# Performance work log

Measured on AMD Instinct MI355X. Metric: run time of the kernel, lower is better.

Reference implementation:

```python
import jax, jax.numpy as jnp
import numpy as np

# ---- static config (mirrors LSSTransform defaults) ----
B, N, CIN, CT = 4, 6, 512, 64
OGH, OGW, DS = 256, 704, 16
FH, FW = OGH // DS, OGW // DS            # 16, 44
DB0, DB1, DBS = 4.0, 45.0, 1.0
D = int((DB1 - DB0) / DBS)               # 41 depth bins
NXX, NYY, NZZ = 128, 128, 1              # BEV grid from x/y/z bounds
DXv = np.array([0.8, 0.8, 20.0], np.float32)            # dx
BXv = np.array([-51.2 + 0.4, -51.2 + 0.4, 0.0], np.float32)  # bx = lower + dx/2


def _frustum():
    # (D, fH, fW, 3) of (pixel_u, pixel_v, depth), as in create_frustum
    ds = np.broadcast_to(np.arange(DB0, DB1, DBS, dtype=np.float32)[:, None, None], (D, FH, FW))
    xs = np.broadcast_to(np.linspace(0, OGW - 1, FW, dtype=np.float32)[None, None, :], (D, FH, FW))
    ys = np.broadcast_to(np.linspace(0, OGH - 1, FH, dtype=np.float32)[None, :, None], (D, FH, FW))
    return jnp.asarray(np.stack([xs, ys, ds], axis=-1))

FRUSTUM = _frustum()


def setup_inputs() -> dict:
    key = jax.random.key(0)
    k0, k1, k2 = jax.random.split(key, 3)
    x = jax.random.normal(k0, (B, N, CIN, FH, FW), jnp.float32)
    # camera->ego rotation: ego = (z_cam, x_cam, y_cam), so depth maps to ego-x
    R = jnp.array([[0., 0., 1.], [1., 0., 0.], [0., 1., 0.]], jnp.float32)
    rots = jnp.broadcast_to(R, (B, N, 3, 3)) + 0.0
    trans = 0.5 * jax.random.normal(k1, (B, N, 3), jnp.float32)
    K = jnp.array([[500., 0., OGW / 2.], [0., 500., OGH / 2.], [0., 0., 1.]], jnp.float32)
    intrins = jnp.broadcast_to(K, (B, N, 3, 3)) + 0.0
    post_rots = jnp.broadcast_to(jnp.eye(3, dtype=jnp.float32), (B, N, 3, 3)) + 0.0
    post_trans = jnp.zeros((B, N, 3), jnp.float32)
    Wd = 0.02 * jax.random.normal(k2, (D + CT, CIN), jnp.float32)  # depthnet 1x1 conv weight
    bd = jnp.zeros((D + CT,), jnp.float32)
    return dict(x=x, rots=rots, trans=trans, intrins=intrins,
                post_rots=post_rots, post_trans=post_trans, Wd=Wd, bd=bd)


def _forward(x, rots, trans, intrins, post_rots, post_trans, Wd, bd):
    # depthnet: 1x1 conv == channel matmul
    feat = jnp.einsum('bnchw,oc->bnohw', x, Wd) + bd[None, None, :, None, None]
    depth = jax.nn.softmax(feat[:, :, :D], axis=2)          # (B,N,D,H,W)
    cvt = feat[:, :, D:D + CT]                              # (B,N,CT,H,W)
    vol = depth[:, :, None] * cvt[:, :, :, None]            # (B,N,CT,D,H,W)
    vol = jnp.transpose(vol, (0, 1, 3, 4, 5, 2))            # (B,N,D,H,W,CT)

    # get_geometry: undo image augs, unproject, cam->ego
    pts = FRUSTUM[None, None] - post_trans[:, :, None, None, None, :]
    pts = jnp.einsum('bnij,bndhwj->bndhwi', jnp.linalg.inv(post_rots), pts)
    pts = jnp.concatenate([pts[..., :2] * pts[..., 2:3], pts[..., 2:3]], axis=-1)
    comb = rots @ jnp.linalg.inv(intrins)
    pts = jnp.einsum('bnij,bndhwj->bndhwi', comb, pts) + trans[:, :, None, None, None, :]

    # voxel_pooling: truncating cast matches torch .long()
    g = ((pts - (jnp.asarray(BXv) - jnp.asarray(DXv) / 2.0)) / jnp.asarray(DXv)).astype(jnp.int32)
    gx, gy, gz = g[..., 0], g[..., 1], g[..., 2]
    kept = (gx >= 0) & (gx < NXX) & (gy >= 0) & (gy < NYY) & (gz >= 0) & (gz < NZZ)
    bix = jnp.arange(B, dtype=jnp.int32)[:, None, None, None, None]
    vox = ((bix * NZZ + gz) * NYY + gy) * NXX + gx          # flat voxel id per point
    TOT = B * NZZ * NYY * NXX
    seg = jnp.where(kept, vox, TOT).reshape(-1)             # invalid -> trash bucket
    feats = vol.reshape(-1, CT)                             # (Nprime, CT)
    sums = jax.ops.segment_sum(feats, seg, num_segments=TOT + 1)[:TOT]
    final = sums.reshape(B, NZZ, NYY, NXX, CT)
    # (B, C, nz, ny, nx) then cat over z into channels -> (B, nz*C, ny, nx)
    final = jnp.transpose(final, (0, 1, 4, 2, 3)).reshape(B, NZZ * CT, NYY, NXX)
    return final


def reference(x, rots, trans, intrins, post_rots, post_trans, Wd, bd):
    return _forward(x, rots, trans, intrins, post_rots, post_trans, Wd, bd)
```

## Files before the change

### kernel.cpp

```cpp
#include <hip/hip_runtime.h>
#include <hip/hip_bf16.h>
#include <math.h>

#define B_   4
#define N_   6
#define CIN  512
#define CT   64
#define Dd   41
#define FH   16
#define FW   44
#define NPIX 704
#define NO   105
#define DSTR 48
#define NXX  128
#define NYY  128
#define NZZ  1
#define TOT  (B_*NZZ*NYY*NXX)
#define NPTS (B_*N_*Dd*NPIX)
#define NCHUNK ((NPTS+63)/64)

#define WSTRIDE 520

#define GEMM_BLOCKS 1056
#define GEOM_BLOCKS 4224

typedef __attribute__((ext_vector_type(8))) short short8;
typedef __attribute__((ext_vector_type(4))) float f32x4;


__device__ __forceinline__ unsigned short f2bf(float f) {
    unsigned u = __float_as_uint(f);
    u += 0x7FFFu + ((u >> 16) & 1u);
    return (unsigned short)(u >> 16);
}

__device__ __forceinline__ void inv3(const double* m, double* o) {
    double a=m[0],b=m[1],c=m[2],d=m[3],e=m[4],f=m[5],g=m[6],h=m[7],i=m[8];
    double A  =  (e*i - f*h);
    double Bc = -(d*i - f*g);
    double Cc =  (d*h - e*g);
    double det = a*A + b*Bc + c*Cc;
    double inv = 1.0/det;
    o[0]=A*inv;            o[1]=-(b*i - c*h)*inv;  o[2]= (b*f - c*e)*inv;
    o[3]=Bc*inv;           o[4]= (a*i - c*g)*inv;  o[5]=-(a*f - c*d)*inv;
    o[6]=Cc*inv;           o[7]=-(a*h - b*g)*inv;  o[8]= (a*e - b*d)*inv;
}

__device__ __forceinline__ void geom_lane(const double* s_tf, int b, int pix, int l,
                                          bool& kept, int& vox) {
    const int hh = pix / FW, ww = pix % FW;
    const double fx = (double)((float)(ww * (703.0/43.0)));
    const double fy = (double)((float)(hh * 17.0));
    const double px = fx - s_tf[21], py = fy - s_tf[22], mz = -s_tf[23];
    const double qx0 = s_tf[ 9]*px + s_tf[10]*py + s_tf[11]*mz, qx1 = s_tf[11];
    const double qy0 = s_tf[12]*px + s_tf[13]*py + s_tf[14]*mz, qy1 = s_tf[14];
    const double qz0 = s_tf[15]*px + s_tf[16]*py + s_tf[17]*mz, qz1 = s_tf[17];
    const double ux0 = s_tf[0]*qx0 + s_tf[1]*qy0 + s_tf[2], ux1 = s_tf[0]*qx1 + s_tf[1]*qy1;
    const double uy0 = s_tf[3]*qx0 + s_tf[4]*qy0 + s_tf[5], uy1 = s_tf[3]*qx1 + s_tf[4]*qy1;
    const double uz0 = s_tf[6]*qx0 + s_tf[7]*qy0 + s_tf[8], uz1 = s_tf[6]*qx1 + s_tf[7]*qy1;
    const double t0 = s_tf[18], t1 = s_tf[19], t2 = s_tf[20];

    const double DXD = (double)0.8f;
    const double LOX = (double)(-50.8f) - DXD*0.5;
    const double LOY = LOX;
    const double DZD = 20.0;
    const double LOZ = -10.0;

    kept = false; vox = 0;
    if (l < Dd) {
        double fz = 4.0 + (double)l;
        double qz = qz0 + qz1*fz;
        double sx = qz*(ux0 + ux1*fz) + t0;
        double sy = qz*(uy0 + uy1*fz) + t1;
        double sz = qz*(uz0 + uz1*fz) + t2;
        int gx = (int)((sx - LOX) / DXD);
        int gy = (int)((sy - LOY) / DXD);
        int gz = (int)((sz - LOZ) / DZD);
        kept = (gx>=0) & (gx<NXX) & (gy>=0) & (gy<NYY) & (gz>=0) & (gz<NZZ);
        vox  = (((b*NZZ + gz)*NYY + gy)*NXX + gx);
    }
}

__global__ __launch_bounds__(256) void prep_kernel(
    const float* __restrict__ rots, const float* __restrict__ trans,
    const float* __restrict__ intrins, const float* __restrict__ post_rots,
    const float* __restrict__ post_trans, const float* __restrict__ Wd,
    const float* __restrict__ x,
    double* __restrict__ tf, unsigned short* __restrict__ WdB,
    unsigned short* __restrict__ xB)
{
    const int t = threadIdx.x;
    if (blockIdx.x < 2112) {
        __shared__ float s_x[64*65];
        const int p    = blockIdx.x;
        const int bn   = p / 88;
        const int r    = p % 88;
        const int kg   = r / 11;
        const int tile = r % 11;
        const int pix0 = tile * 64;

        const float* src = x + ((size_t)bn*CIN + kg*64)*NPIX + pix0;
        #pragma unroll
        for (int i = 0; i < 16; i++) {
            int idx = i*256 + t;
            int k  = idx >> 6;
            int px = idx & 63;
            s_x[k*65 + px] = src[(size_t)k*NPIX + px];
        }
        __syncthreads();

        const int px  = t & 63;
        #pragma unroll
        for (int pass = 0; pass < 2; pass++) {
            int k8l = (t >> 6) + 4*pass;
            unsigned pk[4];
            #pragma unroll
            for (int i = 0; i < 4; i++) {
                float a = s_x[(k8l*8 + 2*i    )*65 + px];
                float c = s_x[(k8l*8 + 2*i + 1)*65 + px];
                pk[i] = (unsigned)f2bf(a) | ((unsigned)f2bf(c) << 16);
            }
            unsigned* dst = (unsigned*)&xB[(((size_t)(bn*64 + kg*8 + k8l))*NPIX + pix0 + px)*8];
            *(uint4*)dst = make_uint4(pk[0], pk[1], pk[2], pk[3]);
        }
    } else {
        int b2 = blockIdx.x - 2112;
        int idx = b2*256 + t;
        if (idx < 128*CIN) {
            int o = idx / CIN;
            WdB[idx] = (o < NO) ? f2bf(Wd[idx]) : (unsigned short)0;
        }
        if (b2 == 0 && t < B_*N_) {
            int bn = t;
            double k[9], pr[9], r[9], ik[9], ipr[9], c[9];
            for (int i=0;i<9;i++) { k[i]=intrins[bn*9+i]; pr[i]=post_rots[bn*9+i]; r[i]=rots[bn*9+i]; }
            inv3(k, ik);
            inv3(pr, ipr);
            for (int i=0;i<3;i++)
                for (int j=0;j<3;j++) {
                    double s = 0.0;
                    for (int kk=0;kk<3;kk++) s += r[i*3+kk]*ik[kk*3+j];
                    c[i*3+j] = s;
                }
            double* o = tf + bn*24;
            for (int i=0;i<9;i++) o[i]   = c[i];
            for (int i=0;i<9;i++) o[9+i] = ipr[i];
            for (int i=0;i<3;i++) o[18+i] = (double)trans[bn*3+i];
            for (int i=0;i<3;i++) o[21+i] = (double)post_trans[bn*3+i];
        }
    }
}

__global__ __launch_bounds__(256) void gemm_geom_kernel(
    const unsigned short* __restrict__ xB, const unsigned short* __restrict__ WdB,
    const float* __restrict__ bd, const double* __restrict__ tf,
    float* __restrict__ featD, float* __restrict__ featB,
    int* __restrict__ hist, int* __restrict__ rank_arr)
{
    __shared__ unsigned short s_wd[32*WSTRIDE];
    __shared__ double s_tf[24];

    const int t    = threadIdx.x;
    const int l    = t & 63;
    const int wv   = t >> 6;

    if (blockIdx.x < GEMM_BLOCKS) {
        const int col  = l & 15;
        const int quad = l >> 4;
        const int xcd = blockIdx.x & 7;
        const int q   = blockIdx.x >> 3;
        const int s   = q & 3;
        const int pg  = q >> 2;
        const int p   = pg*8 + xcd;
        const int bn   = p / 11;
        const int tile = p % 11;
        const int pix0 = tile * 64;

        {
            const int o  = t >> 3;
            const int c8 = t & 7;
            const unsigned short* srcw = WdB + (size_t)(s*32 + o)*CIN;
            #pragma unroll
            for (int i = 0; i < 8; i++) {
                int k = c8*8 + i*64;
                *(uint4*)&s_wd[o*WSTRIDE + k] = *(const uint4*)&srcw[k];
            }
        }
        __syncthreads();

        f32x4 acc[2];
        acc[0] = (f32x4){0.f,0.f,0.f,0.f};
        acc[1] = (f32x4){0.f,0.f,0.f,0.f};

        const int pix = pix0 + wv*16 + col;
        const unsigned short* xbase = xB + (((size_t)(bn*64))*NPIX)*8;

        #pragma unroll
        for (int ks = 0; ks < 16; ks++) {
            const int k8 = ks*4 + quad;
            short8 bfr = *(const short8*)&xbase[((size_t)k8*NPIX + pix)*8];
            #pragma unroll
            for (int j = 0; j < 2; j++) {
                short8 afr = *(const short8*)&s_wd[(j*16 + col)*WSTRIDE + ks*32 + quad*8];
                acc[j] = __builtin_amdgcn_mfma_f32_16x16x32_bf16(afr, bfr, acc[j], 0, 0, 0);
            }
        }

        const size_t prow = (size_t)(bn*NPIX + pix);
        #pragma unroll
        for (int j = 0; j < 2; j++) {
            #pragma unroll
            for (int rr = 0; rr < 4; rr++) {
                int o = (2*s + j)*16 + quad*4 + rr;
                if (o < Dd) {
                    featD[prow*DSTR + o] = acc[j][rr] + bd[o];
                } else if (o < NO) {
                    featB[prow*CT + (o - Dd)] = acc[j][rr] + bd[o];
                }
            }
        }
    } else {
        const int bid2 = blockIdx.x - GEMM_BLOCKS;
        const int bid  = (bid2 & 7) * 528 + (bid2 >> 3);
        const int bn  = bid / 176;
        const int pix = (bid % 176)*4 + wv;
        const int b   = bn / N_;

        if (t < 24) s_tf[t] = tf[bn*24 + t];
        __syncthreads();

        bool kept; int vox;
        geom_lane(s_tf, b, pix, l, kept, vox);
        if (kept) {
            int rank = atomicAdd(&hist[vox], 1);
            rank_arr[(size_t)(bn*NPIX + pix)*Dd + l] = rank;
        }
    }
}

__global__ __launch_bounds__(256) void scan1_kernel(const int* __restrict__ hist,
                                                    int* __restrict__ offs,
                                                    int* __restrict__ bsum) {
    __shared__ int s[256];
    const int t = threadIdx.x;
    const int i = blockIdx.x*256 + t;
    int val = hist[i];
    s[t] = val;
    __syncthreads();
    #pragma unroll
    for (int off = 1; off < 256; off <<= 1) {
        int u = (t >= off) ? s[t-off] : 0;
        __syncthreads();
        s[t] += u;
        __syncthreads();
    }
    offs[i] = s[t] - val;
    if (t == 255) bsum[blockIdx.x] = s[255];
}

__global__ __launch_bounds__(256) void scan2_kernel(int* __restrict__ bsum,
                                                    int* __restrict__ np) {
    __shared__ int s[256];
    const int t = threadIdx.x;
    int v = bsum[t];
    s[t] = v;
    __syncthreads();
    #pragma unroll
    for (int off = 1; off < 256; off <<= 1) {
        int u = (t >= off) ? s[t-off] : 0;
        __syncthreads();
        s[t] += u;
        __syncthreads();
    }
    bsum[t] = s[t] - v;
    if (t == 255) np[0] = s[255];
}

__global__ __launch_bounds__(256) void sm_scatter_kernel(
    const float* __restrict__ featD, const double* __restrict__ tf,
    const int* __restrict__ offs, const int* __restrict__ bsum,
    const int* __restrict__ rank_arr, uint2* __restrict__ rec)
{
    __shared__ double s_tf[24];
    const int bid = (blockIdx.x & 7) * 528 + (blockIdx.x >> 3);
    const int t   = threadIdx.x;
    const int l   = t & 63;
    const int wv  = t >> 6;
    const int bn  = bid / 176;
    const int pix = (bid % 176)*4 + wv;
    const int b   = bn / N_;

    if (t < 24) s_tf[t] = tf[bn*24 + t];
    __syncthreads();

    const size_t prow = (size_t)(bn*NPIX + pix);

    float logit = (l < Dd) ? featD[prow*DSTR + l] : -3.0e38f;
    float mm = logit;
    #pragma unroll
    for (int off = 32; off > 0; off >>= 1) mm = fmaxf(mm, __shfl_xor(mm, off));
    float e = (l < Dd) ? expf(logit - mm) : 0.0f;
    float ssum = e;
    #pragma unroll
    for (int off = 32; off > 0; off >>= 1) ssum += __shfl_xor(ssum, off);
    const float wgt = e / ssum;

    bool kept; int vox;
    geom_lane(s_tf, b, pix, l, kept, vox);
    if (kept) {
        int pos = offs[vox] + bsum[vox >> 8] + rank_arr[prow*Dd + l];
        unsigned pk = ((unsigned)vox << 15) | (unsigned)prow;
        rec[pos] = make_uint2(pk, __float_as_uint(wgt));
    }
}

__global__ __launch_bounds__(256) void gather_kernel(
    const uint2* __restrict__ rec, const int* __restrict__ np,
    const float* __restrict__ featB, float* __restrict__ scat)
{
    const int bid = (blockIdx.x & 7) * 339 + (blockIdx.x >> 3);
    const int t  = threadIdx.x;
    const int wv = t >> 6;
    const int l  = t & 63;
    const int chunk = bid * 4 + wv;
    const int base  = chunk * 64;
    const int Np = np[0];
    if (base >= Np) return;
    int cnt = Np - base; if (cnt > 64) cnt = 64;

    unsigned pk = 0; float w = 0.0f;
    if (l < cnt) { uint2 r = rec[base + l]; pk = r.x; w = __uint_as_float(r.y); }
    unsigned pkm = __shfl(pk, (l == 0) ? 0 : (l - 1));
    unsigned long long starts =
        __ballot((l > 0) && (l < cnt) && ((pk >> 15) != (pkm >> 15)));

    unsigned long long m = starts;
    int rs = 0;
    while (rs < cnt) {
        int re = m ? (__ffsll((unsigned long long)m) - 1) : cnt;
        if (m) m &= m - 1;
        float acc = 0.0f;
        for (int j = rs; j < re; j++) {
            unsigned pkj = __shfl(pk, j);
            float    wj  = __shfl(w, j);
            unsigned id  = pkj & 0x7FFFu;
            acc += wj * featB[(size_t)id * CT + l];
        }
        unsigned vrun = __shfl(pk, rs) >> 15;
        float* dst = scat + (size_t)vrun * CT + l;
        if (rs == 0 || re == cnt) {
            unsafeAtomicAdd(dst, acc);
        } else {
            *dst = acc;
        }
        rs = re;
    }
}

__global__ __launch_bounds__(256) void transpose_k(const float* __restrict__ scat,
                                                   float* __restrict__ out) {
    __shared__ float tile[64][65];
    int b  = blockIdx.x >> 8;
    int t0 = (blockIdx.x & 255) * 64;
    const float* src = scat + (size_t)b * (NYY*NXX) * CT;
    #pragma unroll
    for (int i=0;i<16;i++) {
        int idx = threadIdx.x + i*256;
        int p = idx >> 6, c = idx & 63;
        tile[p][c] = src[(size_t)(t0+p)*CT + c];
    }
    __syncthreads();
    float* dst = out + (size_t)b * CT * (NYY*NXX);
    #pragma unroll
    for (int i=0;i<16;i++) {
        int idx = threadIdx.x + i*256;
        int c = idx >> 6, p = idx & 63;
        dst[(size_t)c*(NYY*NXX) + t0 + p] = tile[p][c];
    }
}

extern "C" void kernel_launch(void* const* d_in, const int* in_sizes, int n_in,
                              void* d_out, int out_size, void* d_ws, size_t ws_size,
                              hipStream_t stream) {
    const float* x          = (const float*)d_in[0];
    const float* rots       = (const float*)d_in[1];
    const float* trans      = (const float*)d_in[2];
    const float* intrins    = (const float*)d_in[3];
    const float* post_rots  = (const float*)d_in[4];
    const float* post_trans = (const float*)d_in[5];
    const float* Wd         = (const float*)d_in[6];
    const float* bd         = (const float*)d_in[7];
    float* out = (float*)d_out;

    char* ws = (char*)d_ws;
    float*          featB  = (float*)ws;          ws += (size_t)B_*N_*NPIX*CT*4;
    float*          featD  = (float*)ws;          ws += (size_t)B_*N_*NPIX*DSTR*4;
    char*           Xreg   = ws;                  ws += (size_t)B_*N_*CIN*NPIX*2;
    int*            rank_a = (int*)ws;            ws += (size_t)NPTS*4;
    uint2*          rec    = (uint2*)ws;          ws += (size_t)NPTS*8;
    int*            hist   = (int*)ws;            ws += (size_t)TOT*4;
    int*            offs   = (int*)ws;            ws += (size_t)TOT*4;
    int*            bsum   = (int*)ws;            ws += 256*4;
    int*            np     = (int*)ws;            ws += 256;
    double*         tf     = (double*)ws;         ws += (size_t)B_*N_*24*8;
    unsigned short* WdB    = (unsigned short*)ws; ws += (size_t)128*CIN*2;

    unsigned short* xB   = (unsigned short*)Xreg;
    float*          scat = (float*)Xreg;

    hipMemsetAsync(hist, 0, (size_t)TOT*4, stream);
    prep_kernel<<<2368, 256, 0, stream>>>(rots, trans, intrins, post_rots, post_trans,
                                          Wd, x, tf, WdB, xB);
    gemm_geom_kernel<<<GEMM_BLOCKS + GEOM_BLOCKS, 256, 0, stream>>>(
        xB, WdB, bd, tf, featD, featB, hist, rank_a);
    hipMemsetAsync(scat, 0, (size_t)TOT*CT*4, stream);
    scan1_kernel<<<TOT/256, 256, 0, stream>>>(hist, offs, bsum);
    scan2_kernel<<<1, 256, 0, stream>>>(bsum, np);
    sm_scatter_kernel<<<B_*N_*176, 256, 0, stream>>>(featD, tf, offs, bsum, rank_a, rec);
    gather_kernel<<<2712, 256, 0, stream>>>(rec, np, featB, scat);
    transpose_k<<<B_*(NYY*NXX/64), 256, 0, stream>>>(scat, out);
}
```

Before: 208.9 us.

## Interleave GEMM and geometry blocks, read weights from global, vectorize prep loads

The fused GEMM and geometry kernel now interleaves one GEMM block per five blocks instead of running all GEMM blocks first, so the compute-bound MFMA work overlaps with the atomic-bound geometry work. The GEMM blocks no longer stage the weight slice in shared memory and read A fragments straight from global or L2, which removes the large LDS allocation and a barrier but adds redundant global loads. The prep transpose now uses float4 loads with a padded stride of 68, and since 64*1056=4224*... mapping bid2 = bidx - bidx/5 - 1 covers geometry blocks exactly (5280 = 1056*5).

```diff
diff --git a/kernel.cpp b/kernel.cpp
--- a/kernel.cpp
+++ b/kernel.cpp
@@ -19,10 +19,9 @@
 #define NPTS (B_*N_*Dd*NPIX)
 #define NCHUNK ((NPTS+63)/64)
 
-#define WSTRIDE 520
-
 #define GEMM_BLOCKS 1056
 #define GEOM_BLOCKS 4224
+#define FUSED_BLOCKS (GEMM_BLOCKS + GEOM_BLOCKS)
 
 typedef __attribute__((ext_vector_type(8))) short short8;
 typedef __attribute__((ext_vector_type(4))) float f32x4;
@@ -91,7 +90,7 @@
 {
     const int t = threadIdx.x;
     if (blockIdx.x < 2112) {
-        __shared__ float s_x[64*65];
+        __shared__ float s_x[64*68];
         const int p    = blockIdx.x;
         const int bn   = p / 88;
         const int r    = p % 88;
@@ -101,11 +100,12 @@
 
         const float* src = x + ((size_t)bn*CIN + kg*64)*NPIX + pix0;
         #pragma unroll
-        for (int i = 0; i < 16; i++) {
+        for (int i = 0; i < 4; i++) {
             int idx = i*256 + t;
-            int k  = idx >> 6;
-            int px = idx & 63;
-            s_x[k*65 + px] = src[(size_t)k*NPIX + px];
+            int k   = idx >> 4;
+            int px4 = (idx & 15) * 4;
+            float4 v = *(const float4*)&src[(size_t)k*NPIX + px4];
+            *(float4*)&s_x[k*68 + px4] = v;
         }
         __syncthreads();
 
@@ -116,8 +116,8 @@
             unsigned pk[4];
             #pragma unroll
             for (int i = 0; i < 4; i++) {
-                float a = s_x[(k8l*8 + 2*i    )*65 + px];
-                float c = s_x[(k8l*8 + 2*i + 1)*65 + px];
+                float a = s_x[(k8l*8 + 2*i    )*68 + px];
+                float c = s_x[(k8l*8 + 2*i + 1)*68 + px];
                 pk[i] = (unsigned)f2bf(a) | ((unsigned)f2bf(c) << 16);
             }
             unsigned* dst = (unsigned*)&xB[(((size_t)(bn*64 + kg*8 + k8l))*NPIX + pix0 + px)*8];
@@ -157,18 +157,19 @@
     float* __restrict__ featD, float* __restrict__ featB,
     int* __restrict__ hist, int* __restrict__ rank_arr)
 {
-    __shared__ unsigned short s_wd[32*WSTRIDE];
     __shared__ double s_tf[24];
 
     const int t    = threadIdx.x;
     const int l    = t & 63;
     const int wv   = t >> 6;
-
-    if (blockIdx.x < GEMM_BLOCKS) {
+    const int bidx = blockIdx.x;
+
+    if (bidx % 5 == 0) {
+        const int gb   = bidx / 5;
         const int col  = l & 15;
         const int quad = l >> 4;
-        const int xcd = blockIdx.x & 7;
-        const int q   = blockIdx.x >> 3;
+        const int xcd = gb & 7;
+        const int q   = gb >> 3;
         const int s   = q & 3;
         const int pg  = q >> 2;
         const int p   = pg*8 + xcd;
@@ -176,34 +177,23 @@
         const int tile = p % 11;
         const int pix0 = tile * 64;
 
-        {
-            const int o  = t >> 3;
-            const int c8 = t & 7;
-            const unsigned short* srcw = WdB + (size_t)(s*32 + o)*CIN;
-            #pragma unroll
-            for (int i = 0; i < 8; i++) {
-                int k = c8*8 + i*64;
-                *(uint4*)&s_wd[o*WSTRIDE + k] = *(const uint4*)&srcw[k];
-            }
-        }
-        __syncthreads();
-
         f32x4 acc[2];
         acc[0] = (f32x4){0.f,0.f,0.f,0.f};
         acc[1] = (f32x4){0.f,0.f,0.f,0.f};
 
         const int pix = pix0 + wv*16 + col;
         const unsigned short* xbase = xB + (((size_t)(bn*64))*NPIX)*8;
+        const unsigned short* wb0 = WdB + (size_t)(s*32 +  0 + col)*CIN + quad*8;
+        const unsigned short* wb1 = WdB + (size_t)(s*32 + 16 + col)*CIN + quad*8;
 
         #pragma unroll
         for (int ks = 0; ks < 16; ks++) {
             const int k8 = ks*4 + quad;
             short8 bfr = *(const short8*)&xbase[((size_t)k8*NPIX + pix)*8];
-            #pragma unroll
-            for (int j = 0; j < 2; j++) {
-                short8 afr = *(const short8*)&s_wd[(j*16 + col)*WSTRIDE + ks*32 + quad*8];
-                acc[j] = __builtin_amdgcn_mfma_f32_16x16x32_bf16(afr, bfr, acc[j], 0, 0, 0);
-            }
+            short8 a0  = *(const short8*)&wb0[ks*32];
+            short8 a1  = *(const short8*)&wb1[ks*32];
+            acc[0] = __builtin_amdgcn_mfma_f32_16x16x32_bf16(a0, bfr, acc[0], 0, 0, 0);
+            acc[1] = __builtin_amdgcn_mfma_f32_16x16x32_bf16(a1, bfr, acc[1], 0, 0, 0);
         }
 
         const size_t prow = (size_t)(bn*NPIX + pix);
@@ -220,7 +210,7 @@
             }
         }
     } else {
-        const int bid2 = blockIdx.x - GEMM_BLOCKS;
+        const int bid2 = bidx - (bidx/5) - 1;
         const int bid  = (bid2 & 7) * 528 + (bid2 >> 3);
         const int bn  = bid / 176;
         const int pix = (bid % 176)*4 + wv;
@@ -411,7 +401,7 @@
     hipMemsetAsync(hist, 0, (size_t)TOT*4, stream);
     prep_kernel<<<2368, 256, 0, stream>>>(rots, trans, intrins, post_rots, post_trans,
                                           Wd, x, tf, WdB, xB);
-    gemm_geom_kernel<<<GEMM_BLOCKS + GEOM_BLOCKS, 256, 0, stream>>>(
+    gemm_geom_kernel<<<FUSED_BLOCKS, 256, 0, stream>>>(
         xB, WdB, bd, tf, featD, featB, hist, rank_a);
     hipMemsetAsync(scat, 0, (size_t)TOT*CT*4, stream);
     scan1_kernel<<<TOT/256, 256, 0, stream>>>(hist, offs, bsum);
```

Result: slower. 216.6 us (+3.7%).

## Fuse bf16 conversion into GEMM, merge scans and memsets into fewer kernels

Applied to the files above, without the earlier changes.

Removes the separate x/Wd-to-bf16 prep pass. The GEMM now loads fp32 x and Wd directly, converts them in registers and stages them in LDS tiles, looping over K in chunks of 64. The hist zeroing moves into prep_kernel, the scat zeroing moves into the scan kernel, and the two scan passes merge into one kernel that uses a last-block atomic counter. This drops several launches and memsets plus a full bf16 copy of x through HBM. In exchange the GEMM reloads fp32 x (now 4 blocks per tile re-read and reconvert it) and adds per-chunk barriers.

```diff
diff --git a/kernel.cpp b/kernel.cpp
--- a/kernel.cpp
+++ b/kernel.cpp
@@ -19,7 +19,8 @@
 #define NPTS (B_*N_*Dd*NPIX)
 #define NCHUNK ((NPTS+63)/64)
 
-#define WSTRIDE 520
+#define XSTRIDE 72
+#define WSTRIDE 72
 
 #define GEMM_BLOCKS 1056
 #define GEOM_BLOCKS 4224
@@ -32,6 +33,10 @@
     unsigned u = __float_as_uint(f);
     u += 0x7FFFu + ((u >> 16) & 1u);
     return (unsigned short)(u >> 16);
+}
+
+__device__ __forceinline__ unsigned pack_bf2(float a, float c) {
+    return (unsigned)f2bf(a) | ((unsigned)f2bf(c) << 16);
 }
 
 __device__ __forceinline__ void inv3(const double* m, double* o) {
@@ -84,53 +89,15 @@
 __global__ __launch_bounds__(256) void prep_kernel(
     const float* __restrict__ rots, const float* __restrict__ trans,
     const float* __restrict__ intrins, const float* __restrict__ post_rots,
-    const float* __restrict__ post_trans, const float* __restrict__ Wd,
-    const float* __restrict__ x,
-    double* __restrict__ tf, unsigned short* __restrict__ WdB,
-    unsigned short* __restrict__ xB)
+    const float* __restrict__ post_trans,
+    double* __restrict__ tf, int* __restrict__ hist, int* __restrict__ counter)
 {
     const int t = threadIdx.x;
-    if (blockIdx.x < 2112) {
-        __shared__ float s_x[64*65];
-        const int p    = blockIdx.x;
-        const int bn   = p / 88;
-        const int r    = p % 88;
-        const int kg   = r / 11;
-        const int tile = r % 11;
-        const int pix0 = tile * 64;
-
-        const float* src = x + ((size_t)bn*CIN + kg*64)*NPIX + pix0;
-        #pragma unroll
-        for (int i = 0; i < 16; i++) {
-            int idx = i*256 + t;
-            int k  = idx >> 6;
-            int px = idx & 63;
-            s_x[k*65 + px] = src[(size_t)k*NPIX + px];
-        }
-        __syncthreads();
-
-        const int px  = t & 63;
-        #pragma unroll
-        for (int pass = 0; pass < 2; pass++) {
-            int k8l = (t >> 6) + 4*pass;
-            unsigned pk[4];
-            #pragma unroll
-            for (int i = 0; i < 4; i++) {
-                float a = s_x[(k8l*8 + 2*i    )*65 + px];
-                float c = s_x[(k8l*8 + 2*i + 1)*65 + px];
-                pk[i] = (unsigned)f2bf(a) | ((unsigned)f2bf(c) << 16);
-            }
-            unsigned* dst = (unsigned*)&xB[(((size_t)(bn*64 + kg*8 + k8l))*NPIX + pix0 + px)*8];
-            *(uint4*)dst = make_uint4(pk[0], pk[1], pk[2], pk[3]);
-        }
+    if (blockIdx.x < 256) {
+        hist[blockIdx.x*256 + t] = 0;
     } else {
-        int b2 = blockIdx.x - 2112;
-        int idx = b2*256 + t;
-        if (idx < 128*CIN) {
-            int o = idx / CIN;
-            WdB[idx] = (o < NO) ? f2bf(Wd[idx]) : (unsigned short)0;
-        }
-        if (b2 == 0 && t < B_*N_) {
+        if (t == 0) counter[0] = 0;
+        if (t < B_*N_) {
             int bn = t;
             double k[9], pr[9], r[9], ik[9], ipr[9], c[9];
             for (int i=0;i<9;i++) { k[i]=intrins[bn*9+i]; pr[i]=post_rots[bn*9+i]; r[i]=rots[bn*9+i]; }
@@ -152,11 +119,12 @@
 }
 
 __global__ __launch_bounds__(256) void gemm_geom_kernel(
-    const unsigned short* __restrict__ xB, const unsigned short* __restrict__ WdB,
+    const float* __restrict__ x, const float* __restrict__ Wd,
     const float* __restrict__ bd, const double* __restrict__ tf,
     float* __restrict__ featD, float* __restrict__ featB,
     int* __restrict__ hist, int* __restrict__ rank_arr)
 {
+    __shared__ unsigned short s_xT[64*XSTRIDE];
     __shared__ unsigned short s_wd[32*WSTRIDE];
     __shared__ double s_tf[24];
 
@@ -176,34 +144,55 @@
         const int tile = p % 11;
         const int pix0 = tile * 64;
 
-        {
-            const int o  = t >> 3;
-            const int c8 = t & 7;
-            const unsigned short* srcw = WdB + (size_t)(s*32 + o)*CIN;
-            #pragma unroll
-            for (int i = 0; i < 8; i++) {
-                int k = c8*8 + i*64;
-                *(uint4*)&s_wd[o*WSTRIDE + k] = *(const uint4*)&srcw[k];
-            }
-        }
-        __syncthreads();
+        const int pix = pix0 + wv*16 + col;
+        const float* xb = x + (size_t)bn * CIN * NPIX + pix0;
+
+        const int wo = t >> 3;
+        const int wc = t & 7;
+        const int og = s*32 + wo;
+        const float* wsrc = Wd + (size_t)og*CIN + wc*8;
 
         f32x4 acc[2];
         acc[0] = (f32x4){0.f,0.f,0.f,0.f};
         acc[1] = (f32x4){0.f,0.f,0.f,0.f};
 
-        const int pix = pix0 + wv*16 + col;
-        const unsigned short* xbase = xB + (((size_t)(bn*64))*NPIX)*8;
-
-        #pragma unroll
-        for (int ks = 0; ks < 16; ks++) {
-            const int k8 = ks*4 + quad;
-            short8 bfr = *(const short8*)&xbase[((size_t)k8*NPIX + pix)*8];
+        for (int k0 = 0; k0 < CIN; k0 += 64) {
+            {
+                unsigned pkx[8];
+                #pragma unroll
+                for (int j = 0; j < 8; j++) {
+                    float a = xb[(size_t)(k0 + wv*16 + 2*j    )*NPIX + l];
+                    float c = xb[(size_t)(k0 + wv*16 + 2*j + 1)*NPIX + l];
+                    pkx[j] = pack_bf2(a, c);
+                }
+                unsigned* dst = (unsigned*)&s_xT[l*XSTRIDE + wv*16];
+                *(uint4*)(dst + 0) = make_uint4(pkx[0],pkx[1],pkx[2],pkx[3]);
+                *(uint4*)(dst + 4) = make_uint4(pkx[4],pkx[5],pkx[6],pkx[7]);
+            }
+            {
+                unsigned pkw[4];
+                if (og < NO) {
+                    const float* wp = wsrc + k0;
+                    #pragma unroll
+                    for (int i = 0; i < 4; i++)
+                        pkw[i] = pack_bf2(wp[2*i], wp[2*i+1]);
+                } else {
+                    pkw[0] = pkw[1] = pkw[2] = pkw[3] = 0u;
+                }
+                *(uint4*)&s_wd[wo*WSTRIDE + wc*8] = make_uint4(pkw[0],pkw[1],pkw[2],pkw[3]);
+            }
+            __syncthreads();
+
             #pragma unroll
-            for (int j = 0; j < 2; j++) {
-                short8 afr = *(const short8*)&s_wd[(j*16 + col)*WSTRIDE + ks*32 + quad*8];
-                acc[j] = __builtin_amdgcn_mfma_f32_16x16x32_bf16(afr, bfr, acc[j], 0, 0, 0);
+            for (int ks = 0; ks < 2; ks++) {
+                short8 bfr = *(const short8*)&s_xT[(wv*16 + col)*XSTRIDE + ks*32 + quad*8];
+                #pragma unroll
+                for (int j = 0; j < 2; j++) {
+                    short8 afr = *(const short8*)&s_wd[(j*16 + col)*WSTRIDE + ks*32 + quad*8];
+                    acc[j] = __builtin_amdgcn_mfma_f32_16x16x32_bf16(afr, bfr, acc[j], 0, 0, 0);
+                }
             }
+            __syncthreads();
         }
 
         const size_t prow = (size_t)(bn*NPIX + pix);
@@ -238,42 +227,56 @@
     }
 }
 
-__global__ __launch_bounds__(256) void scan1_kernel(const int* __restrict__ hist,
-                                                    int* __restrict__ offs,
-                                                    int* __restrict__ bsum) {
+__global__ __launch_bounds__(256) void scan_kernel(const int* __restrict__ hist,
+                                                   int* __restrict__ offs,
+                                                   int* __restrict__ bsum,
+                                                   int* __restrict__ np,
+                                                   int* __restrict__ counter,
+                                                   float4* __restrict__ scat4) {
     __shared__ int s[256];
+    __shared__ int lastdone;
     const int t = threadIdx.x;
     const int i = blockIdx.x*256 + t;
     int val = hist[i];
     s[t] = val;
     __syncthreads();
+
+    {
+        float4 z = make_float4(0.f, 0.f, 0.f, 0.f);
+        float4* dst = scat4 + (size_t)blockIdx.x*4096 + t;
+        #pragma unroll
+        for (int j = 0; j < 16; j++) dst[j*256] = z;
+    }
+
     #pragma unroll
     for (int off = 1; off < 256; off <<= 1) {
+        __syncthreads();
         int u = (t >= off) ? s[t-off] : 0;
         __syncthreads();
         s[t] += u;
-        __syncthreads();
-    }
+    }
+    __syncthreads();
     offs[i] = s[t] - val;
     if (t == 255) bsum[blockIdx.x] = s[255];
-}
-
-__global__ __launch_bounds__(256) void scan2_kernel(int* __restrict__ bsum,
-                                                    int* __restrict__ np) {
-    __shared__ int s[256];
-    const int t = threadIdx.x;
-    int v = bsum[t];
-    s[t] = v;
+
+    __threadfence();
+    if (t == 0) lastdone = (atomicAdd(counter, 1) == 255) ? 1 : 0;
     __syncthreads();
-    #pragma unroll
-    for (int off = 1; off < 256; off <<= 1) {
-        int u = (t >= off) ? s[t-off] : 0;
+    if (lastdone) {
+        __threadfence();
+        int v = bsum[t];
+        s[t] = v;
         __syncthreads();
-        s[t] += u;
-        __syncthreads();
-    }
-    bsum[t] = s[t] - v;
-    if (t == 255) np[0] = s[255];
+        #pragma unroll
+        for (int off = 1; off < 256; off <<= 1) {
+            int u = (t >= off) ? s[t-off] : 0;
+            __syncthreads();
+            s[t] += u;
+            __syncthreads();
+        }
+        bsum[t] = s[t] - v;
+        if (t == 255) np[0] = s[255];
+    }
 }
 
 __global__ __launch_bounds__(256) void sm_scatter_kernel(
@@ -395,27 +398,21 @@
     char* ws = (char*)d_ws;
     float*          featB  = (float*)ws;          ws += (size_t)B_*N_*NPIX*CT*4;
     float*          featD  = (float*)ws;          ws += (size_t)B_*N_*NPIX*DSTR*4;
-    char*           Xreg   = ws;                  ws += (size_t)B_*N_*CIN*NPIX*2;
+    float*          scat   = (float*)ws;          ws += (size_t)TOT*CT*4;
     int*            rank_a = (int*)ws;            ws += (size_t)NPTS*4;
     uint2*          rec    = (uint2*)ws;          ws += (size_t)NPTS*8;
     int*            hist   = (int*)ws;            ws += (size_t)TOT*4;
     int*            offs   = (int*)ws;            ws += (size_t)TOT*4;
     int*            bsum   = (int*)ws;            ws += 256*4;
     int*            np     = (int*)ws;            ws += 256;
+    int*            counter= (int*)ws;            ws += 256;
     double*         tf     = (double*)ws;         ws += (size_t)B_*N_*24*8;
-    unsigned short* WdB    = (unsigned short*)ws; ws += (size_t)128*CIN*2;
-
-    unsigned short* xB   = (unsigned short*)Xreg;
-    float*          scat = (float*)Xreg;
-
-    hipMemsetAsync(hist, 0, (size_t)TOT*4, stream);
-    prep_kernel<<<2368, 256, 0, stream>>>(rots, trans, intrins, post_rots, post_trans,
-                                          Wd, x, tf, WdB, xB);
+
+    prep_kernel<<<257, 256, 0, stream>>>(rots, trans, intrins, post_rots, post_trans,
+                                         tf, hist, counter);
     gemm_geom_kernel<<<GEMM_BLOCKS + GEOM_BLOCKS, 256, 0, stream>>>(
-        xB, WdB, bd, tf, featD, featB, hist, rank_a);
-    hipMemsetAsync(scat, 0, (size_t)TOT*CT*4, stream);
-    scan1_kernel<<<TOT/256, 256, 0, stream>>>(hist, offs, bsum);
-    scan2_kernel<<<1, 256, 0, stream>>>(bsum, np);
+        x, Wd, bd, tf, featD, featB, hist, rank_a);
+    scan_kernel<<<TOT/256, 256, 0, stream>>>(hist, offs, bsum, np, counter, (float4*)scat);
     sm_scatter_kernel<<<B_*N_*176, 256, 0, stream>>>(featD, tf, offs, bsum, rank_a, rec);
     gather_kernel<<<2712, 256, 0, stream>>>(rec, np, featB, scat);
     transpose_k<<<B_*(NYY*NXX/64), 256, 0, stream>>>(scat, out);
```

Measured after the change: 213.6 us. 2.2% more time.
